# Kernel tuning notes

Hardware: AMD Instinct MI355X
Metric: run time of the kernel (lower is better)

The kernel has to match this reference:

```python
import jax, jax.numpy as jnp
import numpy as np
from jax import lax

P = 10          # patch_size
STRIDE_FM = 4   # 2 ** att_depth


def conv2d(x, w, b=None, stride=1, padding=0):
    out = lax.conv_general_dilated(
        x, w, (stride, stride), [(padding, padding), (padding, padding)],
        dimension_numbers=('NCHW', 'OIHW', 'NCHW'))
    if b is not None:
        out = out + b[None, :, None, None]
    return out


def group_norm(x, w, b, groups=2, eps=1e-5):
    B, C, H, W = x.shape
    xg = x.reshape(B, groups, -1)
    m = xg.mean(-1, keepdims=True)
    v = xg.var(-1, keepdims=True)
    xg = (xg - m) * lax.rsqrt(v + eps)
    return xg.reshape(B, C, H, W) * w[None, :, None, None] + b[None, :, None, None]


def pixel_shuffle(x, r):
    B, C, H, W = x.shape
    x = x.reshape(B, C // (r * r), r, r, H, W)
    return x.transpose(0, 1, 4, 2, 5, 3).reshape(B, C // (r * r), H * r, W * r)


def convsc(x, w, b, gw, gb, upsampling):
    # SimVP ConvSC: conv(k=3,s=1,pad=1) [-> PixelShuffle(2) if upsampling] -> GroupNorm(2) -> SiLU
    y = conv2d(x, w, b, stride=1, padding=1)
    if upsampling:
        y = pixel_shuffle(y, 2)
    return jax.nn.silu(group_norm(y, gw, gb))


def unfold_p(x):
    # non-overlapping PxP patches per channel: [B,C,h,w] -> [B,C,P*P,L]
    B, C, h, w = x.shape
    x = x.reshape(B, C, h // P, P, w // P, P)
    return x.transpose(0, 1, 3, 5, 2, 4).reshape(B, C, P * P, (h // P) * (w // P))


def fold_p(x, h, w):
    # exact inverse of unfold_p (stride == kernel, no overlap): [B,C,P*P,L] -> [B,C,h,w]
    B, C, _, L = x.shape
    x = x.reshape(B, C, P, P, h // P, w // P)
    return x.transpose(0, 1, 4, 2, 5, 3).reshape(B, C, h, w)


def setup_inputs() -> dict:
    key = jax.random.key(0)
    ks = jax.random.split(key, 12)
    B, Ch, Co, H, W = 16, 64, 3, 160, 160
    L = (H // P) * (W // P)                      # 256 fold patches over Y
    L2 = (H // (P * STRIDE_FM)) * (W // (P * STRIDE_FM))  # 16 unfold patches over feamap
    s = 0.05
    return {
        'attentions': jax.random.uniform(ks[0], (B, Co, L, L2), jnp.float32),
        'hid': jax.random.normal(ks[1], (B, Ch, H // 4, W // 4), jnp.float32),
        'enc1': jax.random.normal(ks[2], (B, Ch, H, W), jnp.float32),
        'dec0_w': s * jax.random.normal(ks[3], (4 * Ch, Ch, 3, 3), jnp.float32),
        'dec0_b': jnp.zeros((4 * Ch,), jnp.float32),
        'dec0_gw': jnp.ones((Ch,), jnp.float32), 'dec0_gb': jnp.zeros((Ch,), jnp.float32),
        'dec1_w': s * jax.random.normal(ks[4], (Ch, Ch, 3, 3), jnp.float32),
        'dec1_b': jnp.zeros((Ch,), jnp.float32),
        'dec1_gw': jnp.ones((Ch,), jnp.float32), 'dec1_gb': jnp.zeros((Ch,), jnp.float32),
        'dec2_w': s * jax.random.normal(ks[5], (4 * Ch, Ch, 3, 3), jnp.float32),
        'dec2_b': jnp.zeros((4 * Ch,), jnp.float32),
        'dec2_gw': jnp.ones((Ch,), jnp.float32), 'dec2_gb': jnp.zeros((Ch,), jnp.float32),
        'dec3_w': s * jax.random.normal(ks[6], (Ch, Ch, 3, 3), jnp.float32),
        'dec3_b': jnp.zeros((Ch,), jnp.float32),
        'dec3_gw': jnp.ones((Ch,), jnp.float32), 'dec3_gb': jnp.zeros((Ch,), jnp.float32),
        'readout_w': s * jax.random.normal(ks[7], (Co, Ch, 1, 1), jnp.float32),
        'readout_b': jnp.zeros((Co,), jnp.float32),
        'feamap_w': s * jax.random.normal(ks[8], (4, Co, STRIDE_FM, STRIDE_FM), jnp.float32),
    }


def reference(attentions, hid, enc1,
              dec0_w, dec0_b, dec0_gw, dec0_gb,
              dec1_w, dec1_b, dec1_gw, dec1_gb,
              dec2_w, dec2_b, dec2_gw, dec2_gb,
              dec3_w, dec3_b, dec3_gw, dec3_gb,
              readout_w, readout_b, feamap_w):
    # samplings reversed for N_S=4: [True, False, True, False]
    hid = convsc(hid, dec0_w, dec0_b, dec0_gw, dec0_gb, True)
    hid = convsc(hid, dec1_w, dec1_b, dec1_gw, dec1_gb, False)
    hid = convsc(hid, dec2_w, dec2_b, dec2_gw, dec2_gb, True)
    Y = convsc(hid + enc1, dec3_w, dec3_b, dec3_gw, dec3_gb, False)
    Y = conv2d(Y, readout_w, readout_b)                      # [B,3,160,160]

    B, Co, H, W = Y.shape
    argx = conv2d(Y, feamap_w, None, stride=STRIDE_FM) / (STRIDE_FM * STRIDE_FM)  # [B,4,40,40]
    patches = unfold_p(argx[:, :Co])                         # [B,3,100,L2] (all channels batched)
    nz = jnp.count_nonzero(attentions, axis=-1)[..., None].astype(Y.dtype) + 1e-5  # [B,3,L,1]
    att = jnp.einsum('bclk,bcpk->bclp', attentions / nz, patches)  # [B,3,L,100]
    correction = fold_p(att.transpose(0, 1, 3, 2), H, W)     # [B,3,160,160]
    return correction * Y + Y
```

## Files before the change

kernel.cpp:

```cpp
#include <hip/hip_runtime.h>


#define DEVFN static __device__ __forceinline__

typedef short v8s __attribute__((ext_vector_type(8)));
typedef float v4f __attribute__((ext_vector_type(4)));

DEVFN float silu_f(float t) { return t / (1.f + __expf(-t)); }

DEVFN ushort f2bf(float x) {
  union { float f; unsigned u; } t; t.f = x;
  unsigned r = t.u + 0x7FFFu + ((t.u >> 16) & 1u);
  return (ushort)(r >> 16);
}

__global__ void zero_k(float* __restrict__ p, int n) {
  int i = blockIdx.x * 256 + threadIdx.x;
  if (i < n) p[i] = 0.f;
}

template<int OC>
__global__ void repackw_k(const float* __restrict__ src, ushort* __restrict__ dst) {
  int i = blockIdx.x * 256 + threadIdx.x;
  if (i >= OC * 576) return;
  int oc = i / 576, r = i - oc * 576;
  int ic = r / 9, tap = r - ic * 9;
  int kc = tap * 8 + (ic >> 3), j = ic & 7;
  dst[((size_t)kc * OC + oc) * 8 + j] = f2bf(src[i]);
}

template<int HP, int WP>
__global__ void border_k(ushort* __restrict__ outP) {
  int idx = blockIdx.x * 256 + threadIdx.x;
  if (idx >= 16 * HP * WP) return;
  int p = idx % (HP * WP);
  int y = p / WP, x = p - y * WP;
  if (y == 0 || y == HP - 1 || x == 0 || x == WP - 1) {
    uint4 z = {0u, 0u, 0u, 0u};
    uint4* dst = (uint4*)(outP + (size_t)idx * 64);
    #pragma unroll
    for (int k = 0; k < 8; ++k) dst[k] = z;
  }
}

DEVFN void gn_stats(const float* __restrict__ st, int bg, float N,
                    float& mean, float& rstd) {
  float s = 0.f, q = 0.f;
  #pragma unroll
  for (int sl = 0; sl < 8; ++sl) {
    s += st[sl * 64 + bg * 2 + 0];
    q += st[sl * 64 + bg * 2 + 1];
  }
  float m = s / N;
  mean = m;
  rstd = rsqrtf(q / N - m * m + 1e-5f);
}

template<int HW_TOT, int WOUT, int MODE>
__global__ __launch_bounds__(256)
void act_k(const float* __restrict__ in, const float* __restrict__ st,
           const float* __restrict__ gw, const float* __restrict__ gb,
           const float* __restrict__ addsrc, ushort* __restrict__ outP)
{
  constexpr int HOUT = HW_TOT / WOUT;
  constexpr int WP = WOUT + 2, HP = HOUT + 2;
  __shared__ uint4 sT[256 * 8];
  const int tid = threadIdx.x;
  constexpr int NBLK = (HW_TOT + 255) / 256;
  const int b  = blockIdx.x / NBLK;
  const int p0 = (blockIdx.x - b * NBLK) * 256;
  const int px = p0 + tid;

  float mean[2], rstd[2];
  if (MODE >= 1) {
    const float N = 32.f * HW_TOT;
    #pragma unroll
    for (int g = 0; g < 2; ++g) gn_stats(st, b * 2 + g, N, mean[g], rstd[g]);
  }
  if (px < HW_TOT) {
    const float* ip = in + (size_t)b * 64 * HW_TOT + px;
    #pragma unroll 2
    for (int cc = 0; cc < 8; ++cc) {
      unsigned w[4];
      #pragma unroll
      for (int jp = 0; jp < 4; ++jp) {
        float v0, v1;
        #pragma unroll
        for (int h = 0; h < 2; ++h) {
          int c = cc * 8 + jp * 2 + h;
          float v = ip[(size_t)c * HW_TOT];
          if (MODE >= 1) {
            v = silu_f((v - mean[c >> 5]) * rstd[c >> 5] * gw[c] + gb[c]);
            if (MODE == 2) v += addsrc[(size_t)(b * 64 + c) * HW_TOT + px];
          }
          if (h == 0) v0 = v; else v1 = v;
        }
        w[jp] = (unsigned)f2bf(v0) | ((unsigned)f2bf(v1) << 16);
      }
      uint4 pk = {w[0], w[1], w[2], w[3]};
      sT[tid * 8 + (cc ^ (tid & 7))] = pk;
    }
  }
  __syncthreads();
  const int o = tid & 7, pr = tid >> 3;
  #pragma unroll
  for (int i = 0; i < 8; ++i) {
    int p = i * 32 + pr;
    int gpx = p0 + p;
    if (gpx < HW_TOT) {
      int y = gpx / WOUT, x = gpx - y * WOUT;
      uint4 val = sT[p * 8 + (o ^ (p & 7))];
      *(uint4*)(outP + (((size_t)(b * HP) + y + 1) * WP + (x + 1)) * 64 + o * 8) = val;
    }
  }
}


#define FE18(M) M(0) M(1) M(2) M(3) M(4) M(5) M(6) M(7) M(8) M(9) M(10) \
                M(11) M(12) M(13) M(14) M(15) M(16) M(17)

#define WDL(t) \
  v8s Wa##t = ((const v8s*)wrep)[(size_t)((t) * 4 + sub) * OCT + ocbase + lx]; \
  v8s Wb##t = ((const v8s*)wrep)[(size_t)((t) * 4 + sub) * OCT + ocbase + 16 + lx];

#define KST(t) { \
    const int col_ = xb + lx + (((t) >> 1) % 3); \
    v8s b_ = __builtin_bit_cast(v8s, sQ[((rbase + wrow + (t) / 6) * LWS + col_) * 8 + \
                                        (((((t) & 1) * 4 + sub)) ^ (col_ & 7))]); \
    a0 = __builtin_amdgcn_mfma_f32_16x16x32_bf16(Wa##t, b_, a0, 0, 0, 0); \
    a1 = __builtin_amdgcn_mfma_f32_16x16x32_bf16(Wb##t, b_, a1, 0, 0, 0); }

template<int HIN, int WIN, int WT, int NG, int RPB, int OCT, bool PSF,
         int WEU_MIN, int WEU_MAX>
__global__
__attribute__((amdgpu_flat_work_group_size(256, 256),
               amdgpu_waves_per_eu(WEU_MIN, WEU_MAX)))
void convm_k(const uint4* __restrict__ inP, const ushort* __restrict__ wrep,
             const float* __restrict__ bias, float* __restrict__ out,
             float* __restrict__ stp)
{
  constexpr int HP = HIN + 2, WP = WIN + 2;
  constexpr int LH = RPB + 2, LW = WT + 2;
  constexpr int NOCB = OCT / 64;
  constexpr int LRD = (NG * 16 + 2 > LW) ? (NG * 16 + 2) : LW;
  constexpr int LWS = (LRD + 7) & ~7;
  constexpr int NCHUNK = LH * LWS * 8;
  static_assert(NCHUNK % 256 == 0, "staging must tile evenly");
  constexpr int STK = NCHUNK / 256;
  __shared__ uint4 sQ[NCHUNK];
  __shared__ float red[4][2];

  const int tid  = threadIdx.x;
  const int lane = tid & 63;
  const int wave = tid >> 6;
  const int sub  = lane >> 4;
  const int lx   = lane & 15;
  const int wrow = wave >> 1;
  const int b    = blockIdx.y / NOCB;
  const int ocb  = blockIdx.y - b * NOCB;
  constexpr int NTX = WIN / WT;
  const int tx    = blockIdx.x % NTX;
  const int ych   = blockIdx.x / NTX;
  const int x0    = tx * WT;
  const int ybase = ych * RPB;
  const int ocbase = ocb * 64 + (wave & 1) * 32;

  FE18(WDL)

  const v4f bi0 = *(const v4f*)&bias[ocbase + sub * 4];
  const v4f bi1 = *(const v4f*)&bias[ocbase + 16 + sub * 4];

  const uint4* gbase = inP + ((size_t)(b * HP + ybase) * WP + x0) * 8;
  uint4 stg[STK];
  #pragma unroll
  for (int k = 0; k < STK; ++k) {
    int q = tid + k * 256;
    int p = q >> 3, cc = q & 7;
    int r = p / LWS, cx = p - r * LWS;
    stg[k] = gbase[((size_t)r * WP + cx) * 8 + cc];
  }
  #pragma unroll
  for (int k = 0; k < STK; ++k) {
    int q = tid + k * 256;
    int p = q >> 3, cc = q & 7;
    int cx = p - (p / LWS) * LWS;
    sQ[p * 8 + (cc ^ (cx & 7))] = stg[k];
  }
  __syncthreads();

  float sA = 0.f, qA = 0.f;

  for (int it = 0; it < RPB / 2; ++it) {
    const int rbase = it * 2;
    const int y = ybase + rbase + wrow;
    for (int xg = 0; xg < NG; ++xg) {
      const int xb = xg * 16;
      v4f a0 = bi0, a1 = bi1;
      FE18(KST)
      const int x = x0 + xb + lx;
      if ((NG * 16 == WT) || (x < WIN)) {
        #pragma unroll
        for (int s = 0; s < 2; ++s) {
          const v4f a = s ? a1 : a0;
          if (!PSF) {
            #pragma unroll
            for (int j = 0; j < 4; ++j) {
              int oc = ocbase + s * 16 + sub * 4 + j;
              out[((size_t)(b * OCT + oc) * HIN + y) * WIN + x] = a[j];
            }
          } else {
            #pragma unroll
            for (int j = 0; j < 4; ++j) {
              int oc = ocbase + s * 16 + sub * 4 + j;
              int c = oc >> 2, rr = (oc >> 1) & 1, ss = oc & 1;
              out[((size_t)(b * 64 + c) * (2 * HIN) + (2 * y + rr)) * (2 * WIN)
                  + (2 * x + ss)] = a[j];
            }
          }
          #pragma unroll
          for (int j = 0; j < 4; ++j) { sA += a[j]; qA += a[j] * a[j]; }
        }
      }
    }
  }

  #pragma unroll
  for (int o = 32; o >= 1; o >>= 1) {
    sA += __shfl_down(sA, o);
    qA += __shfl_down(qA, o);
  }
  if (lane == 0) { red[wave][0] = sA; red[wave][1] = qA; }
  __syncthreads();
  if (tid == 0) {
    float* basep = stp + ((blockIdx.x ^ blockIdx.y) & 7) * 64;
    if (PSF) {
      int g = ocb >> 1;
      atomicAdd(&basep[(b * 2 + g) * 2 + 0],
                red[0][0] + red[1][0] + red[2][0] + red[3][0]);
      atomicAdd(&basep[(b * 2 + g) * 2 + 1],
                red[0][1] + red[1][1] + red[2][1] + red[3][1]);
    } else {
      atomicAdd(&basep[(b * 2 + 0) * 2 + 0], red[0][0] + red[2][0]);
      atomicAdd(&basep[(b * 2 + 0) * 2 + 1], red[0][1] + red[2][1]);
      atomicAdd(&basep[(b * 2 + 1) * 2 + 0], red[1][0] + red[3][0]);
      atomicAdd(&basep[(b * 2 + 1) * 2 + 1], red[1][1] + red[3][1]);
    }
  }
}

__global__ void readout_k(const float* __restrict__ D, const float* __restrict__ st,
                          const float* __restrict__ gw, const float* __restrict__ gb,
                          const float* __restrict__ rw, const float* __restrict__ rb,
                          float* __restrict__ Y)
{
  int idx = blockIdx.x * 256 + threadIdx.x;
  if (idx >= 16 * 25600) return;
  int b = idx / 25600, pix = idx - b * 25600;
  const float N = 32.f * 25600.f;
  float mean[2], rstd[2];
  #pragma unroll
  for (int g = 0; g < 2; ++g) gn_stats(st, b * 2 + g, N, mean[g], rstd[g]);
  float a0 = rb[0], a1 = rb[1], a2 = rb[2];
  const float* dp = D + (size_t)(b * 64) * 25600 + pix;
  #pragma unroll 4
  for (int c = 0; c < 64; ++c) {
    float x = dp[(size_t)c * 25600];
    float t = (x - mean[c >> 5]) * rstd[c >> 5] * gw[c] + gb[c];
    float v = silu_f(t);
    a0 = fmaf(v, rw[c], a0);
    a1 = fmaf(v, rw[64 + c], a1);
    a2 = fmaf(v, rw[128 + c], a2);
  }
  Y[(size_t)(b * 3 + 0) * 25600 + pix] = a0;
  Y[(size_t)(b * 3 + 1) * 25600 + pix] = a1;
  Y[(size_t)(b * 3 + 2) * 25600 + pix] = a2;
}

__global__ void feamap_k(const float* __restrict__ Y, const float* __restrict__ fw,
                         float* __restrict__ argx)
{
  int idx = blockIdx.x * 256 + threadIdx.x;
  if (idx >= 16 * 3 * 1600) return;
  int b  = idx / (3 * 1600);
  int o  = (idx / 1600) % 3;
  int ij = idx % 1600;
  int i = ij / 40, j = ij - i * 40;
  float s = 0.f;
  #pragma unroll
  for (int c = 0; c < 3; ++c)
    #pragma unroll
    for (int u = 0; u < 4; ++u)
      #pragma unroll
      for (int v = 0; v < 4; ++v)
        s += Y[((size_t)(b * 3 + c) * 160 + (4 * i + u)) * 160 + (4 * j + v)]
             * fw[((o * 3 + c) * 4 + u) * 4 + v];
  argx[idx] = s * (1.f / 16.f);
}

__global__ void nz_k(const float* __restrict__ attn, float* __restrict__ nzinv) {
  int idx = blockIdx.x * 256 + threadIdx.x;
  if (idx >= 16 * 3 * 256) return;
  const float* p = attn + (size_t)idx * 16;
  int c = 0;
  #pragma unroll
  for (int k = 0; k < 16; ++k) c += (p[k] != 0.f);
  nzinv[idx] = 1.f / ((float)c + 1e-5f);
}

__global__ void final_k(const float* __restrict__ Y, const float* __restrict__ attn,
                        const float* __restrict__ nzinv, const float* __restrict__ argx,
                        float* __restrict__ out)
{
  int idx = blockIdx.x * 256 + threadIdx.x;
  if (idx >= 16 * 3 * 25600) return;
  int bc  = idx / 25600;
  int pix = idx - bc * 25600;
  int y = pix / 160, x = pix - y * 160;
  int l  = (y / 10) * 16 + (x / 10);
  int pi = y % 10,  pj = x % 10;
  const float* ar = attn + ((size_t)bc * 256 + l) * 16;
  const float* ax = argx + (size_t)bc * 1600;
  float inv = nzinv[bc * 256 + l];
  float corr = 0.f;
  #pragma unroll
  for (int k = 0; k < 16; ++k)
    corr += ar[k] * ax[((k >> 2) * 10 + pi) * 40 + ((k & 3) * 10 + pj)];
  float yv = Y[idx];
  out[idx] = yv * (1.f + corr * inv);
}

extern "C" void kernel_launch(void* const* d_in, const int* in_sizes, int n_in,
                              void* d_out, int out_size, void* d_ws, size_t ws_size,
                              hipStream_t stream)
{
  const float* attn = (const float*)d_in[0];
  const float* hid  = (const float*)d_in[1];
  const float* enc1 = (const float*)d_in[2];
  const float* d0w  = (const float*)d_in[3];
  const float* d0b  = (const float*)d_in[4];
  const float* d0gw = (const float*)d_in[5];
  const float* d0gb = (const float*)d_in[6];
  const float* d1w  = (const float*)d_in[7];
  const float* d1b  = (const float*)d_in[8];
  const float* d1gw = (const float*)d_in[9];
  const float* d1gb = (const float*)d_in[10];
  const float* d2w  = (const float*)d_in[11];
  const float* d2b  = (const float*)d_in[12];
  const float* d2gw = (const float*)d_in[13];
  const float* d2gb = (const float*)d_in[14];
  const float* d3w  = (const float*)d_in[15];
  const float* d3b  = (const float*)d_in[16];
  const float* d3gw = (const float*)d_in[17];
  const float* d3gb = (const float*)d_in[18];
  const float* rw   = (const float*)d_in[19];
  const float* rb   = (const float*)d_in[20];
  const float* fw   = (const float*)d_in[21];

  float* ws = (float*)d_ws;
  size_t o = 0;
  float* bufA  = ws + o; o += (size_t)16 * 64 * 80 * 80;
  float* bufAp = ws + o; o += (size_t)16 * 82 * 82 * 64 / 2;
  float* bufC  = ws + o; o += (size_t)16 * 64 * 160 * 160;
  float* bufCp = ws + o; o += (size_t)16 * 162 * 162 * 64 / 2;
  float* hidPf = ws + o; o += (size_t)16 * 42 * 42 * 64 / 2;
  float* st    = ws + o; o += 4 * 512;
  float* w0f   = ws + o; o += (size_t)72 * 256 * 8 / 2;
  float* w1f   = ws + o; o += (size_t)72 * 64 * 8 / 2;
  float* w2f   = ws + o; o += (size_t)72 * 256 * 8 / 2;
  float* w3f   = ws + o; o += (size_t)72 * 64 * 8 / 2;

  float*  A    = bufA;
  float*  Bb   = bufA;
  ushort* Ap   = (ushort*)bufAp;
  ushort* Bp   = (ushort*)bufAp;
  float*  Cb   = bufC;
  float*  Db   = bufC;
  ushort* Cp   = (ushort*)bufCp;
  ushort* hidP = (ushort*)hidPf;
  float*  Y    = bufA;
  float*  argx = bufA + (size_t)16 * 3 * 25600;
  float*  nzv  = argx + (size_t)16 * 3 * 1600;
  ushort* wr0  = (ushort*)w0f;
  ushort* wr1  = (ushort*)w1f;
  ushort* wr2  = (ushort*)w2f;
  ushort* wr3  = (ushort*)w3f;

  zero_k<<<8, 256, 0, stream>>>(st, 4 * 512);

  repackw_k<256><<<(256 * 576 + 255) / 256, 256, 0, stream>>>(d0w, wr0);
  repackw_k<64><<<(64 * 576 + 255) / 256, 256, 0, stream>>>(d1w, wr1);
  repackw_k<256><<<(256 * 576 + 255) / 256, 256, 0, stream>>>(d2w, wr2);
  repackw_k<64><<<(64 * 576 + 255) / 256, 256, 0, stream>>>(d3w, wr3);

  border_k<42, 42><<<(16 * 42 * 42 + 255) / 256, 256, 0, stream>>>(hidP);
  border_k<82, 82><<<(16 * 82 * 82 + 255) / 256, 256, 0, stream>>>(Ap);
  border_k<162, 162><<<(16 * 162 * 162 + 255) / 256, 256, 0, stream>>>(Cp);

  act_k<1600, 40, 0><<<16 * 7, 256, 0, stream>>>(hid, nullptr, nullptr, nullptr,
                                                 nullptr, hidP);

  convm_k<40, 40, 40, 3, 10, 256, true, 1, 1>
    <<<dim3(4, 16 * 4), 256, 0, stream>>>((const uint4*)hidP, wr0, d0b, A,
                                          st + 0 * 512);

  act_k<6400, 80, 1><<<16 * 25, 256, 0, stream>>>(A, st + 0 * 512, d0gw, d0gb,
                                                  nullptr, Ap);
  convm_k<80, 80, 16, 1, 10, 64, false, 2, 2>
    <<<dim3(40, 16), 256, 0, stream>>>((const uint4*)Ap, wr1, d1b, Bb,
                                       st + 1 * 512);

  act_k<6400, 80, 1><<<16 * 25, 256, 0, stream>>>(Bb, st + 1 * 512, d1gw, d1gb,
                                                  nullptr, Bp);
  convm_k<80, 80, 16, 1, 10, 256, true, 2, 2>
    <<<dim3(40, 16 * 4), 256, 0, stream>>>((const uint4*)Bp, wr2, d2b, Cb,
                                           st + 2 * 512);

  act_k<25600, 160, 2><<<16 * 100, 256, 0, stream>>>(Cb, st + 2 * 512, d2gw,
                                                     d2gb, enc1, Cp);
  convm_k<160, 160, 16, 1, 10, 64, false, 2, 2>
    <<<dim3(160, 16), 256, 0, stream>>>((const uint4*)Cp, wr3, d3b, Db,
                                        st + 3 * 512);

  readout_k<<<(16 * 25600 + 255) / 256, 256, 0, stream>>>(Db, st + 3 * 512,
      d3gw, d3gb, rw, rb, Y);

  feamap_k<<<(16 * 3 * 1600 + 255) / 256, 256, 0, stream>>>(Y, fw, argx);
  nz_k<<<(16 * 3 * 256 + 255) / 256, 256, 0, stream>>>(attn, nzv);
  final_k<<<(16 * 3 * 25600 + 255) / 256, 256, 0, stream>>>(Y, attn, nzv, argx,
      (float*)d_out);
}
```

Before: 268.8 us.

## Write conv outputs as padded bf16 NHWC and normalize in place

```diff
diff --git a/kernel.cpp b/kernel.cpp
--- a/kernel.cpp
+++ b/kernel.cpp
@@ -12,6 +12,10 @@
   union { float f; unsigned u; } t; t.f = x;
   unsigned r = t.u + 0x7FFFu + ((t.u >> 16) & 1u);
   return (ushort)(r >> 16);
+}
+
+DEVFN float bf2f(unsigned u) {
+  union { unsigned i; float f; } t; t.i = u << 16; return t.f;
 }
 
 __global__ void zero_k(float* __restrict__ p, int n) {
@@ -56,11 +60,9 @@
   rstd = rsqrtf(q / N - m * m + 1e-5f);
 }
 
-template<int HW_TOT, int WOUT, int MODE>
+template<int HW_TOT, int WOUT>
 __global__ __launch_bounds__(256)
-void act_k(const float* __restrict__ in, const float* __restrict__ st,
-           const float* __restrict__ gw, const float* __restrict__ gb,
-           const float* __restrict__ addsrc, ushort* __restrict__ outP)
+void pad_k(const float* __restrict__ in, ushort* __restrict__ outP)
 {
   constexpr int HOUT = HW_TOT / WOUT;
   constexpr int WP = WOUT + 2, HP = HOUT + 2;
@@ -71,12 +73,6 @@
   const int p0 = (blockIdx.x - b * NBLK) * 256;
   const int px = p0 + tid;
 
-  float mean[2], rstd[2];
-  if (MODE >= 1) {
-    const float N = 32.f * HW_TOT;
-    #pragma unroll
-    for (int g = 0; g < 2; ++g) gn_stats(st, b * 2 + g, N, mean[g], rstd[g]);
-  }
   if (px < HW_TOT) {
     const float* ip = in + (size_t)b * 64 * HW_TOT + px;
     #pragma unroll 2
@@ -84,17 +80,8 @@
       unsigned w[4];
       #pragma unroll
       for (int jp = 0; jp < 4; ++jp) {
-        float v0, v1;
-        #pragma unroll
-        for (int h = 0; h < 2; ++h) {
-          int c = cc * 8 + jp * 2 + h;
-          float v = ip[(size_t)c * HW_TOT];
-          if (MODE >= 1) {
-            v = silu_f((v - mean[c >> 5]) * rstd[c >> 5] * gw[c] + gb[c]);
-            if (MODE == 2) v += addsrc[(size_t)(b * 64 + c) * HW_TOT + px];
-          }
-          if (h == 0) v0 = v; else v1 = v;
-        }
+        float v0 = ip[(size_t)(cc * 8 + jp * 2) * HW_TOT];
+        float v1 = ip[(size_t)(cc * 8 + jp * 2 + 1) * HW_TOT];
         w[jp] = (unsigned)f2bf(v0) | ((unsigned)f2bf(v1) << 16);
       }
       uint4 pk = {w[0], w[1], w[2], w[3]};
@@ -115,6 +102,50 @@
   }
 }
 
+template<int HOUT, int WOUT, bool ADD>
+__global__ __launch_bounds__(256)
+void actn_k(ushort* __restrict__ buf, const float* __restrict__ st,
+            const float* __restrict__ gw, const float* __restrict__ gb,
+            const float* __restrict__ addsrc)
+{
+  constexpr int HW = HOUT * WOUT;
+  constexpr int WP = WOUT + 2, HP = HOUT + 2;
+  int idx = blockIdx.x * 256 + threadIdx.x;
+  if (idx >= 16 * HW) return;
+  int b = idx / HW, pix = idx - b * HW;
+  int y = pix / WOUT, x = pix - y * WOUT;
+
+  const float N = 32.f * HW;
+  float mean[2], rstd[2];
+  #pragma unroll
+  for (int g = 0; g < 2; ++g) gn_stats(st, b * 2 + g, N, mean[g], rstd[g]);
+
+  uint4* pv = (uint4*)(buf + (((size_t)(b * HP) + y + 1) * WP + (x + 1)) * 64);
+  const float* ap = ADD ? (addsrc + (size_t)b * 64 * HW + pix) : nullptr;
+
+  #pragma unroll
+  for (int cc = 0; cc < 8; ++cc) {
+    uint4 v = pv[cc];
+    unsigned r[4];
+    #pragma unroll
+    for (int k = 0; k < 4; ++k) {
+      unsigned w = (k == 0) ? v.x : (k == 1) ? v.y : (k == 2) ? v.z : v.w;
+      const int c0 = cc * 8 + k * 2;
+      const int g = c0 >> 5;
+      float f0 = bf2f(w & 0xffffu), f1 = bf2f(w >> 16);
+      float r0 = silu_f((f0 - mean[g]) * rstd[g] * gw[c0] + gb[c0]);
+      float r1 = silu_f((f1 - mean[g]) * rstd[g] * gw[c0 + 1] + gb[c0 + 1]);
+      if (ADD) {
+        r0 += ap[(size_t)c0 * HW];
+        r1 += ap[(size_t)(c0 + 1) * HW];
+      }
+      r[k] = (unsigned)f2bf(r0) | ((unsigned)f2bf(r1) << 16);
+    }
+    uint4 pk = {r[0], r[1], r[2], r[3]};
+    pv[cc] = pk;
+  }
+}
+
 
 #define FE18(M) M(0) M(1) M(2) M(3) M(4) M(5) M(6) M(7) M(8) M(9) M(10) \
                 M(11) M(12) M(13) M(14) M(15) M(16) M(17)
@@ -136,10 +167,12 @@
 __attribute__((amdgpu_flat_work_group_size(256, 256),
                amdgpu_waves_per_eu(WEU_MIN, WEU_MAX)))
 void convm_k(const uint4* __restrict__ inP, const ushort* __restrict__ wrep,
-             const float* __restrict__ bias, float* __restrict__ out,
+             const float* __restrict__ bias, ushort* __restrict__ outP,
              float* __restrict__ stp)
 {
   constexpr int HP = HIN + 2, WP = WIN + 2;
+  constexpr int HPo = PSF ? (2 * HIN + 2) : (HIN + 2);
+  constexpr int WPo = PSF ? (2 * WIN + 2) : (WIN + 2);
   constexpr int LH = RPB + 2, LW = WT + 2;
   constexpr int NOCB = OCT / 64;
   constexpr int LRD = (NG * 16 + 2 > LW) ? (NG * 16 + 2) : LW;
@@ -199,26 +232,32 @@
       FE18(KST)
       const int x = x0 + xb + lx;
       if ((NG * 16 == WT) || (x < WIN)) {
-        #pragma unroll
-        for (int s = 0; s < 2; ++s) {
-          const v4f a = s ? a1 : a0;
-          if (!PSF) {
+        if (!PSF) {
+          const size_t pbase =
+            (((size_t)(b * HPo) + y + 1) * WPo + (x + 1)) * 64 + (wave & 1) * 32;
+          #pragma unroll
+          for (int s = 0; s < 2; ++s) {
+            const v4f a = s ? a1 : a0;
+            uint2 pk;
+            pk.x = (unsigned)f2bf(a[0]) | ((unsigned)f2bf(a[1]) << 16);
+            pk.y = (unsigned)f2bf(a[2]) | ((unsigned)f2bf(a[3]) << 16);
+            *(uint2*)(outP + pbase + s * 16 + sub * 4) = pk;
             #pragma unroll
-            for (int j = 0; j < 4; ++j) {
-              int oc = ocbase + s * 16 + sub * 4 + j;
-              out[((size_t)(b * OCT + oc) * HIN + y) * WIN + x] = a[j];
-            }
-          } else {
+            for (int j = 0; j < 4; ++j) { sA += a[j]; qA += a[j] * a[j]; }
+          }
+        } else {
+          #pragma unroll
+          for (int s = 0; s < 2; ++s) {
+            const v4f a = s ? a1 : a0;
             #pragma unroll
             for (int j = 0; j < 4; ++j) {
               int oc = ocbase + s * 16 + sub * 4 + j;
               int c = oc >> 2, rr = (oc >> 1) & 1, ss = oc & 1;
-              out[((size_t)(b * 64 + c) * (2 * HIN) + (2 * y + rr)) * (2 * WIN)
-                  + (2 * x + ss)] = a[j];
+              outP[(((size_t)(b * HPo) + 2 * y + rr + 1) * WPo
+                    + (2 * x + ss + 1)) * 64 + c] = f2bf(a[j]);
+              sA += a[j]; qA += a[j] * a[j];
             }
           }
-          #pragma unroll
-          for (int j = 0; j < 4; ++j) { sA += a[j]; qA += a[j] * a[j]; }
         }
       }
     }
@@ -248,28 +287,39 @@
   }
 }
 
-__global__ void readout_k(const float* __restrict__ D, const float* __restrict__ st,
-                          const float* __restrict__ gw, const float* __restrict__ gb,
-                          const float* __restrict__ rw, const float* __restrict__ rb,
-                          float* __restrict__ Y)
+__global__ __launch_bounds__(256)
+void readout_k(const ushort* __restrict__ Dp, const float* __restrict__ st,
+               const float* __restrict__ gw, const float* __restrict__ gb,
+               const float* __restrict__ rw, const float* __restrict__ rb,
+               float* __restrict__ Y)
 {
   int idx = blockIdx.x * 256 + threadIdx.x;
   if (idx >= 16 * 25600) return;
   int b = idx / 25600, pix = idx - b * 25600;
+  int y = pix / 160, x = pix - y * 160;
   const float N = 32.f * 25600.f;
   float mean[2], rstd[2];
   #pragma unroll
   for (int g = 0; g < 2; ++g) gn_stats(st, b * 2 + g, N, mean[g], rstd[g]);
+
+  const uint4* p = (const uint4*)(Dp + (((size_t)(b * 162) + y + 1) * 162
+                                        + (x + 1)) * 64);
   float a0 = rb[0], a1 = rb[1], a2 = rb[2];
-  const float* dp = D + (size_t)(b * 64) * 25600 + pix;
-  #pragma unroll 4
-  for (int c = 0; c < 64; ++c) {
-    float x = dp[(size_t)c * 25600];
-    float t = (x - mean[c >> 5]) * rstd[c >> 5] * gw[c] + gb[c];
-    float v = silu_f(t);
-    a0 = fmaf(v, rw[c], a0);
-    a1 = fmaf(v, rw[64 + c], a1);
-    a2 = fmaf(v, rw[128 + c], a2);
+  #pragma unroll
+  for (int cc = 0; cc < 8; ++cc) {
+    uint4 v = p[cc];
+    #pragma unroll
+    for (int k = 0; k < 4; ++k) {
+      unsigned w = (k == 0) ? v.x : (k == 1) ? v.y : (k == 2) ? v.z : v.w;
+      const int c0 = cc * 8 + k * 2;
+      const int g = c0 >> 5;
+      float f0 = bf2f(w & 0xffffu), f1 = bf2f(w >> 16);
+      float v0 = silu_f((f0 - mean[g]) * rstd[g] * gw[c0] + gb[c0]);
+      float v1 = silu_f((f1 - mean[g]) * rstd[g] * gw[c0 + 1] + gb[c0 + 1]);
+      a0 = fmaf(v0, rw[c0], a0);       a0 = fmaf(v1, rw[c0 + 1], a0);
+      a1 = fmaf(v0, rw[64 + c0], a1);  a1 = fmaf(v1, rw[64 + c0 + 1], a1);
+      a2 = fmaf(v0, rw[128 + c0], a2); a2 = fmaf(v1, rw[128 + c0 + 1], a2);
+    }
   }
   Y[(size_t)(b * 3 + 0) * 25600 + pix] = a0;
   Y[(size_t)(b * 3 + 1) * 25600 + pix] = a1;
@@ -359,9 +409,10 @@
   float* ws = (float*)d_ws;
   size_t o = 0;
   float* bufA  = ws + o; o += (size_t)16 * 64 * 80 * 80;
-  float* bufAp = ws + o; o += (size_t)16 * 82 * 82 * 64 / 2;
-  float* bufC  = ws + o; o += (size_t)16 * 64 * 160 * 160;
-  float* bufCp = ws + o; o += (size_t)16 * 162 * 162 * 64 / 2;
+  float* Abff  = ws + o; o += (size_t)16 * 82 * 82 * 64 / 2;
+  float* Bbff  = ws + o; o += (size_t)16 * 82 * 82 * 64 / 2;
+  float* Cbff  = ws + o; o += (size_t)16 * 162 * 162 * 64 / 2;
+  float* Dbff  = ws + o; o += (size_t)16 * 162 * 162 * 64 / 2;
   float* hidPf = ws + o; o += (size_t)16 * 42 * 42 * 64 / 2;
   float* st    = ws + o; o += 4 * 512;
   float* w0f   = ws + o; o += (size_t)72 * 256 * 8 / 2;
@@ -369,13 +420,10 @@
   float* w2f   = ws + o; o += (size_t)72 * 256 * 8 / 2;
   float* w3f   = ws + o; o += (size_t)72 * 64 * 8 / 2;
 
-  float*  A    = bufA;
-  float*  Bb   = bufA;
-  ushort* Ap   = (ushort*)bufAp;
-  ushort* Bp   = (ushort*)bufAp;
-  float*  Cb   = bufC;
-  float*  Db   = bufC;
-  ushort* Cp   = (ushort*)bufCp;
+  ushort* Abf  = (ushort*)Abff;
+  ushort* Bbf  = (ushort*)Bbff;
+  ushort* Cbf  = (ushort*)Cbff;
+  ushort* Dbf  = (ushort*)Dbff;
   ushort* hidP = (ushort*)hidPf;
   float*  Y    = bufA;
   float*  argx = bufA + (size_t)16 * 3 * 25600;
@@ -393,35 +441,35 @@
   repackw_k<64><<<(64 * 576 + 255) / 256, 256, 0, stream>>>(d3w, wr3);
 
   border_k<42, 42><<<(16 * 42 * 42 + 255) / 256, 256, 0, stream>>>(hidP);
-  border_k<82, 82><<<(16 * 82 * 82 + 255) / 256, 256, 0, stream>>>(Ap);
-  border_k<162, 162><<<(16 * 162 * 162 + 255) / 256, 256, 0, stream>>>(Cp);
-
-  act_k<1600, 40, 0><<<16 * 7, 256, 0, stream>>>(hid, nullptr, nullptr, nullptr,
-                                                 nullptr, hidP);
+  border_k<82, 82><<<(16 * 82 * 82 + 255) / 256, 256, 0, stream>>>(Abf);
+  border_k<82, 82><<<(16 * 82 * 82 + 255) / 256, 256, 0, stream>>>(Bbf);
+  border_k<162, 162><<<(16 * 162 * 162 + 255) / 256, 256, 0, stream>>>(Cbf);
+
+  pad_k<1600, 40><<<16 * 7, 256, 0, stream>>>(hid, hidP);
 
   convm_k<40, 40, 40, 3, 10, 256, true, 1, 1>
-    <<<dim3(4, 16 * 4), 256, 0, stream>>>((const uint4*)hidP, wr0, d0b, A,
+    <<<dim3(4, 16 * 4), 256, 0, stream>>>((const uint4*)hidP, wr0, d0b, Abf,
                                           st + 0 * 512);
-
-  act_k<6400, 80, 1><<<16 * 25, 256, 0, stream>>>(A, st + 0 * 512, d0gw, d0gb,
-                                                  nullptr, Ap);
+  actn_k<80, 80, false><<<(16 * 6400 + 255) / 256, 256, 0, stream>>>(
+      Abf, st + 0 * 512, d0gw, d0gb, nullptr);
+
   convm_k<80, 80, 16, 1, 10, 64, false, 2, 2>
-    <<<dim3(40, 16), 256, 0, stream>>>((const uint4*)Ap, wr1, d1b, Bb,
+    <<<dim3(40, 16), 256, 0, stream>>>((const uint4*)Abf, wr1, d1b, Bbf,
                                        st + 1 * 512);
-
-  act_k<6400, 80, 1><<<16 * 25, 256, 0, stream>>>(Bb, st + 1 * 512, d1gw, d1gb,
-                                                  nullptr, Bp);
+  actn_k<80, 80, false><<<(16 * 6400 + 255) / 256, 256, 0, stream>>>(
+      Bbf, st + 1 * 512, d1gw, d1gb, nullptr);
+
   convm_k<80, 80, 16, 1, 10, 256, true, 2, 2>
-    <<<dim3(40, 16 * 4), 256, 0, stream>>>((const uint4*)Bp, wr2, d2b, Cb,
+    <<<dim3(40, 16 * 4), 256, 0, stream>>>((const uint4*)Bbf, wr2, d2b, Cbf,
                                            st + 2 * 512);
-
-  act_k<25600, 160, 2><<<16 * 100, 256, 0, stream>>>(Cb, st + 2 * 512, d2gw,
-                                                     d2gb, enc1, Cp);
+  actn_k<160, 160, true><<<(16 * 25600 + 255) / 256, 256, 0, stream>>>(
+      Cbf, st + 2 * 512, d2gw, d2gb, enc1);
+
   convm_k<160, 160, 16, 1, 10, 64, false, 2, 2>
-    <<<dim3(160, 16), 256, 0, stream>>>((const uint4*)Cp, wr3, d3b, Db,
+    <<<dim3(160, 16), 256, 0, stream>>>((const uint4*)Cbf, wr3, d3b, Dbf,
                                         st + 3 * 512);
 
-  readout_k<<<(16 * 25600 + 255) / 256, 256, 0, stream>>>(Db, st + 3 * 512,
+  readout_k<<<(16 * 25600 + 255) / 256, 256, 0, stream>>>(Dbf, st + 3 * 512,
       d3gw, d3gb, rw, rb, Y);
 
   feamap_k<<<(16 * 3 * 1600 + 255) / 256, 256, 0, stream>>>(Y, fw, argx);
```

Result: slower. 339.4 us (+26.3%).
